# Kernel tuning notes

Measured on AMD Instinct MI355X. Metric: run time of the kernel, lower is better.

The kernel has to match this reference:

```python
import jax, jax.numpy as jnp
import numpy as np

B, T, C = 2, 2048, 1024
H, HD = 16, 64
M = 256  # per memory bank
K_CANON = 4


def setup_inputs() -> dict:
    key = jax.random.key(0)
    ks = jax.random.split(key, 10)
    s = 0.02
    return {
        "x": jax.random.normal(ks[0], (B, T, C), jnp.float32),
        "fwd_mem": jax.random.normal(ks[1], (B, M, C), jnp.float32),
        "rev_mem": jax.random.normal(ks[2], (B, M, C), jnp.float32),
        "Wq": jax.random.normal(ks[3], (C, C), jnp.float32) * s,
        "Wk": jax.random.normal(ks[4], (C, C), jnp.float32) * s,
        "Wv": jax.random.normal(ks[5], (C, C), jnp.float32) * s,
        "Wo": jax.random.normal(ks[6], (C, C), jnp.float32) * s,
        "gate_w": jax.random.normal(ks[7], (H, C), jnp.float32) * s,
        "gate_b": jnp.zeros((H,), jnp.float32),
        "canon_w": jax.random.normal(ks[8], (C, 1, K_CANON), jnp.float32) * s,
        "canon_bias": jax.random.normal(ks[9], (C,), jnp.float32) * s,
    }


def _canon_conv(y, canon_w, canon_bias):
    # causal depthwise conv1d with residual; torch weight [C,1,K] -> WIO kernel [K,1,C]
    kern = jnp.transpose(canon_w, (2, 1, 0))
    y_pad = jnp.pad(y, ((0, 0), (K_CANON - 1, 0), (0, 0)))
    conv = jax.lax.conv_general_dilated(
        y_pad, kern, window_strides=(1,), padding='VALID',
        dimension_numbers=('NWC', 'WIO', 'NWC'), feature_group_count=C)
    return y + conv + canon_bias


def reference(x, fwd_mem, rev_mem, Wq, Wk, Wv, Wo, gate_w, gate_b, canon_w, canon_bias):
    Bn, Tn, Cn = x.shape
    scale = 1.0 / np.sqrt(HD)

    q = x @ Wq.T  # [B,T,C]
    k = x @ Wk.T
    v = x @ Wv.T
    # memory integration: project memories with same k/v proj, concat on seq dim
    k = jnp.concatenate([k, fwd_mem @ Wk.T, rev_mem @ Wk.T], axis=1)  # [B,S,C]
    v = jnp.concatenate([v, fwd_mem @ Wv.T, rev_mem @ Wv.T], axis=1)
    S = k.shape[1]
    mem_len = S - Tn

    def heads(t):
        return t.reshape(Bn, -1, H, HD).transpose(0, 2, 1, 3)  # [B,h,S,hd]

    qh, kh, vh = heads(q), heads(k), heads(v)
    scores = jnp.einsum('bhtd,bhsd->bhts', qh, kh) * scale  # [B,h,T,S]
    # causal mask over the first T key columns; memory columns fully visible
    causal = jnp.triu(jnp.ones((Tn, Tn), bool), k=1)
    full_mask = jnp.pad(causal, ((0, 0), (0, mem_len)))  # [T,S]
    scores = jnp.where(full_mask[None, None], -jnp.inf, scores)
    w = jax.nn.softmax(scores, axis=-1)

    # split chunk vs memory, gate memory contribution per head
    w_chunk, w_mem = w[..., :Tn], w[..., Tn:]
    v_chunk, v_mem = vh[:, :, :Tn], vh[:, :, Tn:]
    Y_chunk = jnp.einsum('bhts,bhsd->bhtd', w_chunk, v_chunk)
    Y_mem = jnp.einsum('bhtm,bhmd->bhtd', w_mem, v_mem)
    g = jax.nn.sigmoid(q @ gate_w.T + gate_b)  # [B,T,h]
    g = g.transpose(0, 2, 1)[..., None]  # [B,h,T,1]
    Y = Y_chunk + g * Y_mem

    attn_out = Y.transpose(0, 2, 1, 3).reshape(Bn, Tn, Cn)
    attn_out = _canon_conv(attn_out, canon_w, canon_bias)
    return attn_out @ Wo.T
```

## Files before the change

kernel.cpp:

```cpp
#include <hip/hip_runtime.h>
#include <hip/hip_bf16.h>
#include <cstdint>


typedef __bf16 bf16x8_t __attribute__((ext_vector_type(8)));
typedef __bf16 bf16x4_t __attribute__((ext_vector_type(4)));
typedef float f32x4_t __attribute__((ext_vector_type(4)));

__device__ __forceinline__ f32x4_t mfma16(bf16x8_t a, bf16x8_t b, f32x4_t c) {
    return __builtin_amdgcn_mfma_f32_16x16x32_bf16(a, b, c, 0, 0, 0);
}

__device__ __forceinline__ void gl2lds16(const void* g, void* l) {
    __builtin_amdgcn_global_load_lds(
        (__attribute__((address_space(1))) uint32_t*)(uintptr_t)g,
        (__attribute__((address_space(3))) uint32_t*)l, 16, 0, 0);
}

#define OFF_X   0
#define OFF_FWD 4194304
#define OFF_REV 4718592
#define OFF_WQ  5242880
#define OFF_WK  6291456
#define OFF_WV  7340032
#define OFF_WO  8388608
#define OFF_GW  9437184
#define OFF_GB  9453568
#define OFF_CW  9453584
#define OFF_CB  9457680
#define N_TOT   9458704

__global__ __launch_bounds__(256) void conv_all_kernel(
    const void* p0, const void* p1, const void* p2, const void* p3,
    const void* p4, const void* p5, const void* p6, const void* p7,
    const void* p8, const void* p9, const void* p10,
    __hip_bfloat16* __restrict__ arena)
{
    const int i = (blockIdx.x * 256 + threadIdx.x) * 4;
    if (i >= N_TOT) return;
    const void* src; int off;
    if      (i < OFF_FWD) { src = p0;  off = OFF_X;   }
    else if (i < OFF_REV) { src = p1;  off = OFF_FWD; }
    else if (i < OFF_WQ)  { src = p2;  off = OFF_REV; }
    else if (i < OFF_WK)  { src = p3;  off = OFF_WQ;  }
    else if (i < OFF_WV)  { src = p4;  off = OFF_WK;  }
    else if (i < OFF_WO)  { src = p5;  off = OFF_WV;  }
    else if (i < OFF_GW)  { src = p6;  off = OFF_WO;  }
    else if (i < OFF_GB)  { src = p7;  off = OFF_GW;  }
    else if (i < OFF_CW)  { src = p8;  off = OFF_GB;  }
    else if (i < OFF_CB)  { src = p9;  off = OFF_CW;  }
    else                  { src = p10; off = OFF_CB;  }
    const int j = i - off;
    const float4 f = *(const float4*)((const float*)src + j);
    arena[i + 0] = __float2bfloat16(f.x);
    arena[i + 1] = __float2bfloat16(f.y);
    arena[i + 2] = __float2bfloat16(f.z);
    arena[i + 3] = __float2bfloat16(f.w);
}

__device__ __forceinline__ void gemm_core(
    const __hip_bfloat16* __restrict__ A, const __hip_bfloat16* __restrict__ B,
    void* __restrict__ C, int ldc, int f32o, int arow0, int brow0,
    __hip_bfloat16* As, __hip_bfloat16* Bs)
{
    const int tid  = threadIdx.x;
    const int lane = tid & 63;
    const int wid  = tid >> 6;
    const int q4   = lane >> 4;
    const int c16  = lane & 15;
    const int wm   = (wid >> 1) * 64;
    const int wn   = (wid & 1) * 64;
    const int c0 = tid;
    const int c1 = tid + 256;
    const __hip_bfloat16* gA0 = A + (size_t)(arow0 + (c0 >> 2)) * 1024 + ((c0 & 3) << 3);
    const __hip_bfloat16* gA1 = A + (size_t)(arow0 + (c1 >> 2)) * 1024 + ((c1 & 3) << 3);
    const __hip_bfloat16* gB0 = B + (size_t)(brow0 + (c0 >> 2)) * 1024 + ((c0 & 3) << 3);
    const __hip_bfloat16* gB1 = B + (size_t)(brow0 + (c1 >> 2)) * 1024 + ((c1 & 3) << 3);

    f32x4_t acc[4][4];
#pragma unroll
    for (int i = 0; i < 4; ++i)
#pragma unroll
        for (int j = 0; j < 4; ++j)
#pragma unroll
            for (int r = 0; r < 4; ++r) acc[i][j][r] = 0.0f;

    gl2lds16(gA0, As + c0 * 8);
    gl2lds16(gA1, As + c1 * 8);
    gl2lds16(gB0, Bs + c0 * 8);
    gl2lds16(gB1, Bs + c1 * 8);

    for (int it = 0; it < 32; ++it) {
        __hip_bfloat16* curA = As + (it & 1) * 4096;
        __hip_bfloat16* curB = Bs + (it & 1) * 4096;
        __syncthreads();
        if (it < 31) {
            const int nk = (it + 1) * 32;
            __hip_bfloat16* nA = As + ((it + 1) & 1) * 4096;
            __hip_bfloat16* nB = Bs + ((it + 1) & 1) * 4096;
            gl2lds16(gA0 + nk, nA + c0 * 8);
            gl2lds16(gA1 + nk, nA + c1 * 8);
            gl2lds16(gB0 + nk, nB + c0 * 8);
            gl2lds16(gB1 + nk, nB + c1 * 8);
        }
        bf16x8_t af[4], bfr[4];
#pragma unroll
        for (int i = 0; i < 4; ++i)
            af[i] = *(const bf16x8_t*)&curA[(wm + i * 16 + c16) * 32 + q4 * 8];
#pragma unroll
        for (int j = 0; j < 4; ++j)
            bfr[j] = *(const bf16x8_t*)&curB[(wn + j * 16 + c16) * 32 + q4 * 8];
#pragma unroll
        for (int i = 0; i < 4; ++i)
#pragma unroll
            for (int j = 0; j < 4; ++j)
                acc[i][j] = mfma16(af[i], bfr[j], acc[i][j]);
    }
#pragma unroll
    for (int i = 0; i < 4; ++i) {
        const int mg = arow0 + wm + i * 16 + q4 * 4;
#pragma unroll
        for (int j = 0; j < 4; ++j) {
            const int ng = brow0 + wn + j * 16 + c16;
#pragma unroll
            for (int r = 0; r < 4; ++r) {
                const size_t idx = (size_t)(mg + r) * ldc + ng;
                if (f32o) ((float*)C)[idx] = acc[i][j][r];
                else ((__hip_bfloat16*)C)[idx] = __float2bfloat16(acc[i][j][r]);
            }
        }
    }
}

__global__ __launch_bounds__(256) void qkv_kernel(
    const __hip_bfloat16* __restrict__ x, const __hip_bfloat16* __restrict__ Wqk,
    const __hip_bfloat16* __restrict__ Wv,
    __hip_bfloat16* __restrict__ QK, __hip_bfloat16* __restrict__ Vt)
{
    __shared__ __align__(16) __hip_bfloat16 As[2 * 128 * 32];
    __shared__ __align__(16) __hip_bfloat16 Bs[2 * 128 * 32];
    int id = (blockIdx.x & 7) * 112 + (blockIdx.x >> 3);
    if (id < 512)
        gemm_core(x, Wqk, QK, 2048, 0, (id >> 4) * 128, (id & 15) * 128, As, Bs);
    else if (id < 576) {
        id -= 512;
        gemm_core(x, Wqk, QK, 2048, 0, (32 + (id >> 3)) * 128, (8 + (id & 7)) * 128, As, Bs);
    } else {
        id -= 576;
        gemm_core(Wv, x, Vt, 5120, 0, (id & 7) * 128, (id >> 3) * 128, As, Bs);
    }
}

__global__ __launch_bounds__(256) void gemm_bt_kernel(
    const __hip_bfloat16* __restrict__ A, const __hip_bfloat16* __restrict__ B,
    void* __restrict__ C, int ldc, int f32o)
{
    __shared__ __align__(16) __hip_bfloat16 As[2 * 128 * 32];
    __shared__ __align__(16) __hip_bfloat16 Bs[2 * 128 * 32];
    const int swz = (blockIdx.x & 7) * 32 + (blockIdx.x >> 3);
    const int arow = swz & 31;
    const int brow = swz >> 5;
    gemm_core(A, B, C, ldc, f32o, arow * 128, brow * 128, As, Bs);
}

__global__ __launch_bounds__(64) void gate_kernel(
    const __hip_bfloat16* __restrict__ QK, const __hip_bfloat16* __restrict__ gw,
    const __hip_bfloat16* __restrict__ gb, float* __restrict__ G)
{
    const int base = blockIdx.x * 16;
    const int lane = threadIdx.x;
    const int q4   = lane >> 4;
    const int c16  = lane & 15;
    f32x4_t acc = {0.0f, 0.0f, 0.0f, 0.0f};
    const __hip_bfloat16* qrow = QK + (size_t)(base + c16) * 2048 + q4 * 8;
    const __hip_bfloat16* wrow = gw + (size_t)c16 * 1024 + q4 * 8;
#pragma unroll
    for (int kk = 0; kk < 32; ++kk) {
        const bf16x8_t a = *(const bf16x8_t*)(qrow + kk * 32);
        const bf16x8_t w = *(const bf16x8_t*)(wrow + kk * 32);
        acc = mfma16(a, w, acc);
    }
    const float bias = __bfloat162float(gb[c16]);
#pragma unroll
    for (int r = 0; r < 4; ++r) {
        const int row = base + q4 * 4 + r;
        G[(size_t)row * 16 + c16] = 1.0f / (1.0f + __expf(-(acc[r] + bias)));
    }
}

__global__ __launch_bounds__(256, 4) void attn_kernel(
    const __hip_bfloat16* __restrict__ QK,
    const __hip_bfloat16* __restrict__ Vt,
    const float* __restrict__ G, __hip_bfloat16* __restrict__ Y)
{
    __shared__ __align__(16) __hip_bfloat16 Ks[2][64 * 64];
    __shared__ __align__(16) __hip_bfloat16 Vs[64 * 64];
    __shared__ __align__(16) __hip_bfloat16 Plds[4][16 * 64];
    const int flat = blockIdx.x;
    const int bh   = flat & 31;
    const int tIdx = 31 - (flat >> 5);
    const int b    = bh >> 4;
    const int h    = bh & 15;
    const int tid  = threadIdx.x;
    const int wid  = tid >> 6;
    const int lane = tid & 63;
    const int q4   = lane >> 4;
    const int c16  = lane & 15;
    const int rowbase = tIdx * 64 + wid * 16;

    const __hip_bfloat16* qrow = QK + (size_t)(b * 2048 + rowbase + c16) * 2048 + h * 64;
    const bf16x8_t qa0 = *(const bf16x8_t*)(qrow + q4 * 8);
    const bf16x8_t qa1 = *(const bf16x8_t*)(qrow + 32 + q4 * 8);

    bf16x8_t ones;
#pragma unroll
    for (int i = 0; i < 8; ++i) ones[i] = (__bf16)1.0f;

    float gate[4];
    f32x4_t acc[4];
    f32x4_t rsC = {0.0f, 0.0f, 0.0f, 0.0f};
    f32x4_t rsM = {0.0f, 0.0f, 0.0f, 0.0f};
#pragma unroll
    for (int fp = 0; fp < 4; ++fp)
#pragma unroll
        for (int r = 0; r < 4; ++r) acc[fp][r] = 0.0f;
#pragma unroll
    for (int r = 0; r < 4; ++r)
        gate[r] = G[(size_t)(b * 2048 + rowbase + q4 * 4 + r) * 16 + h];

    const int nCausal = tIdx + 1;
    const int nTiles  = nCausal + 8;
    auto kvRow = [&](int tile) -> int {
        if (tile < nCausal) return b * 2048 + tile * 64;
        const int mi = (tile - nCausal) * 64;
        return (mi < 256) ? 4096 + b * 256 + mi : 4608 + b * 256 + (mi - 256);
    };

    const int srow0 = tid >> 3,         sch0 = (tid & 7) ^ (srow0 & 7);
    const int srow1 = (tid + 256) >> 3, sch1 = (tid & 7) ^ (srow1 & 7);
    const int sw0 = (q4 ^ (c16 & 7)) * 8;
    const int sw1 = ((q4 + 4) ^ (c16 & 7)) * 8;
    const __hip_bfloat16* Kbase = QK + 1024 + h * 64;

    {
        const int vr0 = kvRow(0);
        gl2lds16(Kbase + (size_t)(vr0 + srow0) * 2048 + sch0 * 8, &Ks[0][tid * 8]);
        gl2lds16(Kbase + (size_t)(vr0 + srow1) * 2048 + sch1 * 8, &Ks[0][(tid + 256) * 8]);
    }

    const float SCL = 0.18033688f;

    for (int tile = 0; tile < nTiles; ++tile) {
        const int cur = tile & 1;
        const int vr  = kvRow(tile);
        __syncthreads();
        gl2lds16(Vt + (size_t)(h * 64 + srow0) * 5120 + vr + sch0 * 8, &Vs[tid * 8]);
        gl2lds16(Vt + (size_t)(h * 64 + srow1) * 5120 + vr + sch1 * 8, &Vs[(tid + 256) * 8]);
        if (tile + 1 < nTiles) {
            const int nr = kvRow(tile + 1);
            gl2lds16(Kbase + (size_t)(nr + srow0) * 2048 + sch0 * 8, &Ks[cur ^ 1][tid * 8]);
            gl2lds16(Kbase + (size_t)(nr + srow1) * 2048 + sch1 * 8, &Ks[cur ^ 1][(tid + 256) * 8]);
        }
        const bool isMem  = (tile >= nCausal);
        const bool isDiag = (tile == nCausal - 1);
        bf16x8_t kb0[4], kb1[4];
#pragma unroll
        for (int f = 0; f < 4; ++f) {
            kb0[f] = *(const bf16x8_t*)&Ks[cur][(f * 16 + c16) * 64 + sw0];
            kb1[f] = *(const bf16x8_t*)&Ks[cur][(f * 16 + c16) * 64 + sw1];
        }
        f32x4_t sc[4];
        __builtin_amdgcn_s_setprio(1);
#pragma unroll
        for (int f = 0; f < 4; ++f) {
            f32x4_t z = {0.0f, 0.0f, 0.0f, 0.0f};
            z = mfma16(qa0, kb0[f], z);
            z = mfma16(qa1, kb1[f], z);
            sc[f] = z;
        }
        __builtin_amdgcn_s_setprio(0);
#pragma unroll
        for (int f = 0; f < 4; ++f)
#pragma unroll
            for (int r = 0; r < 4; ++r) {
                float p = __builtin_amdgcn_exp2f(sc[f][r] * SCL);
                if (isDiag) {
                    const int sg = f * 16 + c16;
                    if (sg > wid * 16 + q4 * 4 + r) p = 0.0f;
                }
                if (isMem) p *= gate[r];
                const int prow = q4 * 4 + r;
                const int pcol = f * 16 + c16;
                Plds[wid][prow * 64 + (((pcol >> 3) ^ (prow & 7)) << 3) + (pcol & 7)] =
                    __float2bfloat16(p);
            }
        __syncthreads();
        bf16x8_t vb0[4], vb1[4];
#pragma unroll
        for (int f = 0; f < 4; ++f) {
            vb0[f] = *(const bf16x8_t*)&Vs[(f * 16 + c16) * 64 + sw0];
            vb1[f] = *(const bf16x8_t*)&Vs[(f * 16 + c16) * 64 + sw1];
        }
        const bf16x8_t pa0 = *(const bf16x8_t*)&Plds[wid][c16 * 64 + sw0];
        const bf16x8_t pa1 = *(const bf16x8_t*)&Plds[wid][c16 * 64 + sw1];
        __builtin_amdgcn_s_setprio(1);
        if (isMem) {
            rsM = mfma16(pa0, ones, rsM);
            rsM = mfma16(pa1, ones, rsM);
        } else {
            rsC = mfma16(pa0, ones, rsC);
            rsC = mfma16(pa1, ones, rsC);
        }
#pragma unroll
        for (int fp = 0; fp < 4; ++fp) {
            acc[fp] = mfma16(pa0, vb0[fp], acc[fp]);
            acc[fp] = mfma16(pa1, vb1[fp], acc[fp]);
        }
        __builtin_amdgcn_s_setprio(0);
    }

    float inv[4];
#pragma unroll
    for (int r = 0; r < 4; ++r)
        inv[r] = gate[r] / fmaf(gate[r], rsC[r], rsM[r]);
#pragma unroll
    for (int fp = 0; fp < 4; ++fp)
#pragma unroll
        for (int r = 0; r < 4; ++r) {
            const int tg = rowbase + q4 * 4 + r;
            Y[(size_t)(b * 2048 + tg) * 1024 + h * 64 + fp * 16 + c16] =
                __float2bfloat16(acc[fp][r] * inv[r]);
        }
}

__global__ __launch_bounds__(256) void canon_kernel(
    const __hip_bfloat16* __restrict__ Yin, const __hip_bfloat16* __restrict__ cw,
    const __hip_bfloat16* __restrict__ cb, __hip_bfloat16* __restrict__ Yout)
{
    const int idx = (blockIdx.x * 256 + threadIdx.x) * 4;
    const int c = idx & 1023;
    const int t = (idx >> 10) & 2047;
    const bf16x4_t y0 = *(const bf16x4_t*)(Yin + idx);
    const bf16x4_t bb = *(const bf16x4_t*)(cb + c);
    float a[4];
#pragma unroll
    for (int i = 0; i < 4; ++i) a[i] = (float)y0[i] + (float)bb[i];
    const bf16x8_t w01 = *(const bf16x8_t*)(cw + c * 4);
    const bf16x8_t w23 = *(const bf16x8_t*)(cw + c * 4 + 8);
#pragma unroll
    for (int j = 0; j < 4; ++j) {
        if (t - 3 + j >= 0) {
            const bf16x4_t yj = *(const bf16x4_t*)(Yin + idx + (j - 3) * 1024);
            a[0] += (float)yj[0] * (float)w01[j];
            a[1] += (float)yj[1] * (float)w01[4 + j];
            a[2] += (float)yj[2] * (float)w23[j];
            a[3] += (float)yj[3] * (float)w23[4 + j];
        }
    }
    bf16x4_t o;
#pragma unroll
    for (int i = 0; i < 4; ++i) o[i] = (__bf16)a[i];
    *(bf16x4_t*)(Yout + idx) = o;
}

extern "C" void kernel_launch(void* const* d_in, const int* in_sizes, int n_in,
                              void* d_out, int out_size, void* d_ws, size_t ws_size,
                              hipStream_t stream)
{
    char* ws = (char*)d_ws;
    const size_t MB = 1ull << 20;
    if (ws_size < 50 * MB) return;

    __hip_bfloat16* arena = (__hip_bfloat16*)ws;
    __hip_bfloat16* QK    = (__hip_bfloat16*)(ws + 19 * MB);
    __hip_bfloat16* Vt    = (__hip_bfloat16*)(ws + 39 * MB);
    float*          G     = (float*)(ws + 49 * MB);
    __hip_bfloat16* Y1    = (__hip_bfloat16*)ws;
    __hip_bfloat16* Y2    = QK;

    const dim3 blk(256);
    conv_all_kernel<<<dim3((N_TOT / 4 + 255) / 256), blk, 0, stream>>>(
        d_in[0], d_in[1], d_in[2], d_in[3], d_in[4], d_in[5], d_in[6],
        d_in[7], d_in[8], d_in[9], d_in[10], arena);

    const __hip_bfloat16* xB  = arena + OFF_X;
    const __hip_bfloat16* WqB = arena + OFF_WQ;
    const __hip_bfloat16* WvB = arena + OFF_WV;
    const __hip_bfloat16* WoB = arena + OFF_WO;

    qkv_kernel<<<dim3(896), blk, 0, stream>>>(xB, WqB, WvB, QK, Vt);
    gate_kernel<<<dim3(256), dim3(64), 0, stream>>>(QK, arena + OFF_GW, arena + OFF_GB, G);
    attn_kernel<<<dim3(1024), blk, 0, stream>>>(QK, Vt, G, Y1);
    canon_kernel<<<dim3(4096), blk, 0, stream>>>(Y1, arena + OFF_CW, arena + OFF_CB, Y2);
    gemm_bt_kernel<<<dim3(256), blk, 0, stream>>>(Y2, WoB, d_out, 1024, 1);
}
```

Measured before the change: 232.7 us.

## Fuse gate projection into attention kernel and reuse rows in canon conv

Drops the separate gate kernel. Each attention wave now computes its per-head sigmoid gate with an MFMA over the full query row and spreads the values across lanes with shuffles, overlapping this with the first K tile prefetch. This removes a launch and the G buffer round trip, but every (b,h) block recomputes the gate dot product for its own head, so the full Q rows are re-read across heads. The canon conv kernel now has each thread produce four consecutive time steps from seven loaded rows, cutting redundant loads and shrinking the grid to a quarter.

```diff
diff --git a/kernel.cpp b/kernel.cpp
--- a/kernel.cpp
+++ b/kernel.cpp
@@ -163,35 +163,12 @@
     gemm_core(A, B, C, ldc, f32o, arow * 128, brow * 128, As, Bs);
 }
 
-__global__ __launch_bounds__(64) void gate_kernel(
-    const __hip_bfloat16* __restrict__ QK, const __hip_bfloat16* __restrict__ gw,
-    const __hip_bfloat16* __restrict__ gb, float* __restrict__ G)
-{
-    const int base = blockIdx.x * 16;
-    const int lane = threadIdx.x;
-    const int q4   = lane >> 4;
-    const int c16  = lane & 15;
-    f32x4_t acc = {0.0f, 0.0f, 0.0f, 0.0f};
-    const __hip_bfloat16* qrow = QK + (size_t)(base + c16) * 2048 + q4 * 8;
-    const __hip_bfloat16* wrow = gw + (size_t)c16 * 1024 + q4 * 8;
-#pragma unroll
-    for (int kk = 0; kk < 32; ++kk) {
-        const bf16x8_t a = *(const bf16x8_t*)(qrow + kk * 32);
-        const bf16x8_t w = *(const bf16x8_t*)(wrow + kk * 32);
-        acc = mfma16(a, w, acc);
-    }
-    const float bias = __bfloat162float(gb[c16]);
-#pragma unroll
-    for (int r = 0; r < 4; ++r) {
-        const int row = base + q4 * 4 + r;
-        G[(size_t)row * 16 + c16] = 1.0f / (1.0f + __expf(-(acc[r] + bias)));
-    }
-}
-
 __global__ __launch_bounds__(256, 4) void attn_kernel(
     const __hip_bfloat16* __restrict__ QK,
     const __hip_bfloat16* __restrict__ Vt,
-    const float* __restrict__ G, __hip_bfloat16* __restrict__ Y)
+    const __hip_bfloat16* __restrict__ gw,
+    const __hip_bfloat16* __restrict__ gb,
+    __hip_bfloat16* __restrict__ Y)
 {
     __shared__ __align__(16) __hip_bfloat16 Ks[2][64 * 64];
     __shared__ __align__(16) __hip_bfloat16 Vs[64 * 64];
@@ -208,26 +185,6 @@
     const int c16  = lane & 15;
     const int rowbase = tIdx * 64 + wid * 16;
 
-    const __hip_bfloat16* qrow = QK + (size_t)(b * 2048 + rowbase + c16) * 2048 + h * 64;
-    const bf16x8_t qa0 = *(const bf16x8_t*)(qrow + q4 * 8);
-    const bf16x8_t qa1 = *(const bf16x8_t*)(qrow + 32 + q4 * 8);
-
-    bf16x8_t ones;
-#pragma unroll
-    for (int i = 0; i < 8; ++i) ones[i] = (__bf16)1.0f;
-
-    float gate[4];
-    f32x4_t acc[4];
-    f32x4_t rsC = {0.0f, 0.0f, 0.0f, 0.0f};
-    f32x4_t rsM = {0.0f, 0.0f, 0.0f, 0.0f};
-#pragma unroll
-    for (int fp = 0; fp < 4; ++fp)
-#pragma unroll
-        for (int r = 0; r < 4; ++r) acc[fp][r] = 0.0f;
-#pragma unroll
-    for (int r = 0; r < 4; ++r)
-        gate[r] = G[(size_t)(b * 2048 + rowbase + q4 * 4 + r) * 16 + h];
-
     const int nCausal = tIdx + 1;
     const int nTiles  = nCausal + 8;
     auto kvRow = [&](int tile) -> int {
@@ -247,6 +204,40 @@
         gl2lds16(Kbase + (size_t)(vr0 + srow0) * 2048 + sch0 * 8, &Ks[0][tid * 8]);
         gl2lds16(Kbase + (size_t)(vr0 + srow1) * 2048 + sch1 * 8, &Ks[0][(tid + 256) * 8]);
     }
+
+    float gate[4];
+    {
+        const __hip_bfloat16* qg  = QK + (size_t)(b * 2048 + rowbase + c16) * 2048 + q4 * 8;
+        const __hip_bfloat16* gwp = gw + (size_t)h * 1024 + q4 * 8;
+        f32x4_t gacc = {0.0f, 0.0f, 0.0f, 0.0f};
+#pragma unroll
+        for (int kk = 0; kk < 32; ++kk) {
+            const bf16x8_t ga = *(const bf16x8_t*)(gwp + kk * 32);
+            const bf16x8_t qb = *(const bf16x8_t*)(qg + kk * 32);
+            gacc = mfma16(ga, qb, gacc);
+        }
+        const float gbh = __bfloat162float(gb[h]);
+        const float gself = 1.0f / (1.0f + __expf(-(gacc[0] + gbh)));
+#pragma unroll
+        for (int r = 0; r < 4; ++r)
+            gate[r] = __shfl(gself, (lane & 48) | (q4 * 4 + r), 64);
+    }
+
+    const __hip_bfloat16* qrow = QK + (size_t)(b * 2048 + rowbase + c16) * 2048 + h * 64;
+    const bf16x8_t qa0 = *(const bf16x8_t*)(qrow + q4 * 8);
+    const bf16x8_t qa1 = *(const bf16x8_t*)(qrow + 32 + q4 * 8);
+
+    bf16x8_t ones;
+#pragma unroll
+    for (int i = 0; i < 8; ++i) ones[i] = (__bf16)1.0f;
+
+    f32x4_t acc[4];
+    f32x4_t rsC = {0.0f, 0.0f, 0.0f, 0.0f};
+    f32x4_t rsM = {0.0f, 0.0f, 0.0f, 0.0f};
+#pragma unroll
+    for (int fp = 0; fp < 4; ++fp)
+#pragma unroll
+        for (int r = 0; r < 4; ++r) acc[fp][r] = 0.0f;
 
     const float SCL = 0.18033688f;
 
@@ -337,30 +328,43 @@
     const __hip_bfloat16* __restrict__ Yin, const __hip_bfloat16* __restrict__ cw,
     const __hip_bfloat16* __restrict__ cb, __hip_bfloat16* __restrict__ Yout)
 {
-    const int idx = (blockIdx.x * 256 + threadIdx.x) * 4;
-    const int c = idx & 1023;
-    const int t = (idx >> 10) & 2047;
-    const bf16x4_t y0 = *(const bf16x4_t*)(Yin + idx);
-    const bf16x4_t bb = *(const bf16x4_t*)(cb + c);
-    float a[4];
-#pragma unroll
-    for (int i = 0; i < 4; ++i) a[i] = (float)y0[i] + (float)bb[i];
-    const bf16x8_t w01 = *(const bf16x8_t*)(cw + c * 4);
-    const bf16x8_t w23 = *(const bf16x8_t*)(cw + c * 4 + 8);
-#pragma unroll
-    for (int j = 0; j < 4; ++j) {
-        if (t - 3 + j >= 0) {
-            const bf16x4_t yj = *(const bf16x4_t*)(Yin + idx + (j - 3) * 1024);
-            a[0] += (float)yj[0] * (float)w01[j];
-            a[1] += (float)yj[1] * (float)w01[4 + j];
-            a[2] += (float)yj[2] * (float)w23[j];
-            a[3] += (float)yj[3] * (float)w23[4 + j];
-        }
-    }
-    bf16x4_t o;
-#pragma unroll
-    for (int i = 0; i < 4; ++i) o[i] = (__bf16)a[i];
-    *(bf16x4_t*)(Yout + idx) = o;
+    const int gid = blockIdx.x * 256 + threadIdx.x;
+    const int cc  = (gid & 255) * 4;
+    const int t4  = ((gid >> 8) & 511) * 4;
+    const int b   = gid >> 17;
+    const size_t base = ((size_t)(b * 2048 + t4)) * 1024 + cc;
+
+    bf16x4_t y[7];
+#pragma unroll
+    for (int m = 0; m < 7; ++m) {
+        if (t4 - 3 + m >= 0)
+            y[m] = *(const bf16x4_t*)(Yin + base + (ptrdiff_t)(m - 3) * 1024);
+        else {
+            y[m][0] = (__bf16)0.0f; y[m][1] = (__bf16)0.0f;
+            y[m][2] = (__bf16)0.0f; y[m][3] = (__bf16)0.0f;
+        }
+    }
+    const bf16x8_t w01 = *(const bf16x8_t*)(cw + cc * 4);
+    const bf16x8_t w23 = *(const bf16x8_t*)(cw + cc * 4 + 8);
+    const bf16x4_t bb  = *(const bf16x4_t*)(cb + cc);
+
+#pragma unroll
+    for (int k = 0; k < 4; ++k) {
+        float a[4];
+#pragma unroll
+        for (int i = 0; i < 4; ++i) a[i] = (float)y[k + 3][i] + (float)bb[i];
+#pragma unroll
+        for (int j = 0; j < 4; ++j) {
+            a[0] += (float)y[k + j][0] * (float)w01[j];
+            a[1] += (float)y[k + j][1] * (float)w01[4 + j];
+            a[2] += (float)y[k + j][2] * (float)w23[j];
+            a[3] += (float)y[k + j][3] * (float)w23[4 + j];
+        }
+        bf16x4_t o;
+#pragma unroll
+        for (int i = 0; i < 4; ++i) o[i] = (__bf16)a[i];
+        *(bf16x4_t*)(Yout + base + (size_t)k * 1024) = o;
+    }
 }
 
 extern "C" void kernel_launch(void* const* d_in, const int* in_sizes, int n_in,
@@ -374,7 +378,6 @@
     __hip_bfloat16* arena = (__hip_bfloat16*)ws;
     __hip_bfloat16* QK    = (__hip_bfloat16*)(ws + 19 * MB);
     __hip_bfloat16* Vt    = (__hip_bfloat16*)(ws + 39 * MB);
-    float*          G     = (float*)(ws + 49 * MB);
     __hip_bfloat16* Y1    = (__hip_bfloat16*)ws;
     __hip_bfloat16* Y2    = QK;
 
@@ -389,8 +392,7 @@
     const __hip_bfloat16* WoB = arena + OFF_WO;
 
     qkv_kernel<<<dim3(896), blk, 0, stream>>>(xB, WqB, WvB, QK, Vt);
-    gate_kernel<<<dim3(256), dim3(64), 0, stream>>>(QK, arena + OFF_GW, arena + OFF_GB, G);
-    attn_kernel<<<dim3(1024), blk, 0, stream>>>(QK, Vt, G, Y1);
-    canon_kernel<<<dim3(4096), blk, 0, stream>>>(Y1, arena + OFF_CW, arena + OFF_CB, Y2);
+    attn_kernel<<<dim3(1024), blk, 0, stream>>>(QK, Vt, arena + OFF_GW, arena + OFF_GB, Y1);
+    canon_kernel<<<dim3(1024), blk, 0, stream>>>(Y1, arena + OFF_CW, arena + OFF_CB, Y2);
     gemm_bt_kernel<<<dim3(256), blk, 0, stream>>>(Y2, WoB, d_out, 1024, 1);
 }
```

Result: slower. 240.5 us (+3.4%).
